# Optimization experiments

Measured on AMD Instinct MI355X. Metric: run time of the kernel, lower is better.

## Reference

```python
import jax, jax.numpy as jnp
import numpy as np

VOCAB, EMB, CAP, T, B, H, NC = 50000, 200, 3, 500, 128, 256, 6


def lstm_layer(x_seq, W, b):
    """TF LSTMCell (forget_bias=1.0, tanh) over x_seq [T,B,D] -> hs [T,B,H]."""
    Hh = b.shape[0] // 4
    Bn = x_seq.shape[1]
    def step(carry, x):
        c, h = carry
        z = jnp.concatenate([x, h], axis=-1) @ W + b  # [B,4H]
        i, j, f, o = jnp.split(z, 4, axis=-1)         # TF gate order i,j,f,o
        c = jax.nn.sigmoid(f + 1.0) * c + jax.nn.sigmoid(i) * jnp.tanh(j)
        h = jax.nn.sigmoid(o) * jnp.tanh(c)
        return (c, h), h
    init = (jnp.zeros((Bn, Hh), x_seq.dtype), jnp.zeros((Bn, Hh), x_seq.dtype))
    _, hs = jax.lax.scan(step, init, x_seq)
    return hs


def stack3(x_seq, Ws, bs):
    h = x_seq
    for W, b in zip(Ws, bs):  # fixed 3 layers
        h = lstm_layer(h, W, b)
    return h


def setup_inputs() -> dict:
    key = jax.random.key(0)
    ks = jax.random.split(key, 16)
    s = 0.05
    inp = {
        "words": jax.random.randint(ks[0], (B, T), 0, VOCAB, dtype=jnp.int32),
        "capitals": jax.random.randint(ks[1], (B, T), 0, 4, dtype=jnp.int32),
        "embed_words": jax.random.normal(ks[2], (VOCAB, EMB), jnp.float32) * s,
        "cap_table": jnp.concatenate([jnp.eye(CAP, dtype=jnp.float32),
                                       jnp.zeros((1, CAP), jnp.float32)], 0),
    }
    D0 = EMB + CAP + H  # 459
    D1 = H + H          # 512
    names = [("Wf0", D0), ("Wf1", D1), ("Wf2", D1), ("Wb0", D0), ("Wb1", D1), ("Wb2", D1)]
    for i, (nm, d) in enumerate(names):
        inp[nm] = jax.random.normal(ks[3 + i], (d, 4 * H), jnp.float32) * s
        inp["b" + nm[1:]] = jnp.zeros((4 * H,), jnp.float32)
    inp["d1_W"] = jax.random.normal(ks[10], (2 * H, 64), jnp.float32) * s
    inp["d1_b"] = jnp.zeros((64,), jnp.float32)
    inp["d2_W"] = jax.random.normal(ks[11], (64, NC), jnp.float32) * s
    inp["d2_b"] = jnp.zeros((NC,), jnp.float32)
    return inp


def reference(words, capitals, embed_words, cap_table,
              Wf0, bf0, Wf1, bf1, Wf2, bf2,
              Wb0, bb0, Wb1, bb1, Wb2, bb2,
              d1_W, d1_b, d2_W, d2_b):
    # embed + concat -> [B,T,203], then time-major [T,B,203]
    x = jnp.concatenate([embed_words[words], cap_table[capitals]], axis=-1)
    x = jnp.transpose(x, (1, 0, 2))
    hf = stack3(x, (Wf0, Wf1, Wf2), (bf0, bf1, bf2))                     # [T,B,H]
    hb = stack3(x[::-1], (Wb0, Wb1, Wb2), (bb0, bb1, bb2))[::-1]         # [T,B,H]
    rnn_out = jnp.max(jnp.concatenate([hf, hb], axis=-1), axis=0)        # [B,2H]
    h1 = jax.nn.elu(rnn_out @ d1_W + d1_b)
    return jax.nn.sigmoid(h1 @ d2_W + d2_b)                              # [B,NC]
```

## Files before the change

### kernel.cpp

```cpp
#include <hip/hip_runtime.h>
#include <stdint.h>

#define TSTEPS 500
#define NB 128
#define NH 256
#define RINGN 8

typedef _Float16 f16;
typedef _Float16 f16x8 __attribute__((ext_vector_type(8)));
typedef float f32x4 __attribute__((ext_vector_type(4)));
typedef unsigned long long u64;
typedef unsigned int u32;

static constexpr size_t HSLOT = (size_t)NB*NH;
static constexpr size_t SZ_XCAT  = (size_t)TSTEPS*NB*256*2;
static constexpr size_t SZ_WLDS  = (size_t)6*4*256*256*2;
static constexpr size_t SZ_WREG  = (size_t)6*4*4*4*8*64*8*2;
static constexpr size_t SZ_BIAS  = (size_t)6*4*256*4;
static constexpr size_t SZ_HNEXT = (size_t)6*RINGN*HSLOT*2;
static constexpr size_t SZ_HLOC  = (size_t)6*RINGN*HSLOT*2;
static constexpr size_t SZ_FLAG  = (size_t)6*(TSTEPS+1)*16*4;
static constexpr size_t SZ_DONE  = 256;
static constexpr size_t SZ_RNN   = (size_t)NB*512*4;
static constexpr size_t OFF_XCAT  = 0;
static constexpr size_t OFF_WLDS  = OFF_XCAT + SZ_XCAT;
static constexpr size_t OFF_WREG  = OFF_WLDS + SZ_WLDS;
static constexpr size_t OFF_BIAS  = OFF_WREG + SZ_WREG;
static constexpr size_t OFF_HNEXT = OFF_BIAS + SZ_BIAS;
static constexpr size_t OFF_HLOC  = OFF_HNEXT + SZ_HNEXT;
static constexpr size_t OFF_FLAGL = OFF_HLOC + SZ_HLOC;
static constexpr size_t OFF_FLAGN = OFF_FLAGL + SZ_FLAG;
static constexpr size_t OFF_DONE  = OFF_FLAGN + SZ_FLAG;
static constexpr size_t OFF_RNN   = (OFF_DONE + SZ_DONE + 255) & ~(size_t)255;
static constexpr size_t WS_NEED   = OFF_RNN + SZ_RNN;

__global__ void embed_kernel(const int* __restrict__ words,
                             const int* __restrict__ caps,
                             const float* __restrict__ emb,
                             const float* __restrict__ capt,
                             f16* __restrict__ xcat) {
  int t = blockIdx.x >> 7, b = blockIdx.x & 127, k = threadIdx.x;
  int w  = words[b*TSTEPS + t];
  int cp = caps [b*TSTEPS + t];
  float v = 0.f;
  if (k < 200)      v = emb[(size_t)w*200 + k];
  else if (k < 203) v = capt[cp*3 + (k-200)];
  xcat[((size_t)t*NB + b)*256 + k] = (f16)v;
}

__global__ void pack_kernel(const float* __restrict__ Wf0, const float* __restrict__ bf0,
                            const float* __restrict__ Wf1, const float* __restrict__ bf1,
                            const float* __restrict__ Wf2, const float* __restrict__ bf2,
                            const float* __restrict__ Wb0, const float* __restrict__ bb0,
                            const float* __restrict__ Wb1, const float* __restrict__ bb1,
                            const float* __restrict__ Wb2, const float* __restrict__ bb2,
                            f16* __restrict__ wlds, f16* __restrict__ wreg,
                            float* __restrict__ bias) {
  int bid = blockIdx.x;
  int layer;
  const float* W; const float* bb;
  int part1 = (bid < 6144);
  if (part1) layer = bid >> 10;
  else       layer = (bid - 6144) >> 6;
  switch (layer) {
    case 0: W = Wf0; bb = bf0; break;
    case 1: W = Wf1; bb = bf1; break;
    case 2: W = Wf2; bb = bf2; break;
    case 3: W = Wb0; bb = bb0; break;
    case 4: W = Wb1; bb = bb1; break;
    default: W = Wb2; bb = bb2; break;
  }
  int level = layer % 3;
  if (part1) {
    int ug = (bid >> 8) & 3;
    int n = bid & 255;
    int g = n >> 6, u = n & 63;
    int col = g*256 + ug*64 + u;
    if (threadIdx.x == 0)
      bias[(size_t)(layer*4 + ug)*256 + n] = bb[col] + (g == 2 ? 1.f : 0.f);
    int k = threadIdx.x;
    int row = (level == 0) ? ((k < 203) ? k : -1) : k;
    float v = (row < 0) ? 0.f : W[(size_t)row*1024 + col];
    int idx = (((k >> 3) ^ (n & 7)) << 3) | (k & 7);
    wlds[((size_t)(layer*4 + ug)*256 + n)*256 + idx] = (f16)v;
  } else {
    int r2 = (bid - 6144) & 63;
    int ug = r2 >> 4, wv = (r2 >> 2) & 3, g = r2 & 3;
    int lane = threadIdx.x & 63;
    int col = g*256 + ug*64 + wv*16 + (lane & 15);
    int rbase = (level == 0) ? 203 : 256;
    for (int ks = threadIdx.x >> 6; ks < 8; ks += 4) {
      size_t base = ((((size_t)(layer*4 + ug)*4 + wv)*4 + g)*8 + ks)*512 + (size_t)lane*8;
      #pragma unroll
      for (int j = 0; j < 8; ++j) {
        int k = ks*32 + ((lane >> 4)*8) + j;
        wreg[base + j] = (f16)W[(size_t)(rbase + k)*1024 + col];
      }
    }
  }
}

__global__ void init_kernel(int* __restrict__ flagL, int* __restrict__ flagN,
                            f16* __restrict__ hnext, int* __restrict__ done) {
  int i = blockIdx.x*256 + threadIdx.x;
  if (i < 6*(TSTEPS+1)*16) {
    int t = (i >> 4) % (TSTEPS+1);
    flagL[i] = 0;
    flagN[i] = (t == 0) ? 9 : 0;
  }
  if (i < 98304) {
    int l = i >> 14, e = i & 16383;
    ((u32*)(hnext + (size_t)l*RINGN*HSLOT))[e] = 0u;
  }
  if (i == 0) *done = 0;
}

__device__ __forceinline__ int poll_agent(const int* q) {
  int v;
  for (;;) {
    v = __hip_atomic_load(q, __ATOMIC_RELAXED, __HIP_MEMORY_SCOPE_AGENT);
    if (__all(v != 0)) break;
    __builtin_amdgcn_s_sleep(1);
  }
  return v;
}
__device__ __forceinline__ int ld_flag_l(const int* p) {
  int v;
  asm volatile("global_load_dword %0, %1, off sc0\n\ts_waitcnt vmcnt(0)"
               : "=v"(v) : "v"(p) : "memory");
  return v;
}
__device__ __forceinline__ f16x8 ld_a_l(const f16* p) {
  f16x8 v;
  asm volatile("global_load_dwordx4 %0, %1, off sc0" : "=v"(v) : "v"(p));
  return v;
}
__device__ __forceinline__ f16x8 ld_a_p(const f16* p) {
  f16x8 v;
  asm volatile("global_load_dwordx4 %0, %1, off" : "=v"(v) : "v"(p));
  return v;
}
__device__ __forceinline__ f16x8 ldA_coh(const f16* p) {
  union { u64 q[2]; f16x8 v; } u;
  u.q[0] = __hip_atomic_load((const u64*)p,     __ATOMIC_RELAXED, __HIP_MEMORY_SCOPE_AGENT);
  u.q[1] = __hip_atomic_load((const u64*)p + 1, __ATOMIC_RELAXED, __HIP_MEMORY_SCOPE_AGENT);
  return u.v;
}
__device__ __forceinline__ void st_h_l(f16* p, short s) {
  asm volatile("global_store_short %0, %1, off" :: "v"(p), "v"((int)s) : "memory");
}
__device__ __forceinline__ void st_flag_plain(int* p, int v) {
  asm volatile("global_store_dword %0, %1, off" :: "v"(p), "v"(v) : "memory");
}
__device__ __forceinline__ void vm_wait(int n) {
  if (n == 0)      asm volatile("s_waitcnt vmcnt(0)" ::: "memory");
  else if (n == 8) asm volatile("s_waitcnt vmcnt(8)" ::: "memory");
  __builtin_amdgcn_sched_barrier(0);
}
__device__ __forceinline__ float sigf(float x) {
  return __builtin_amdgcn_rcpf(1.f + __expf(-x));
}
__device__ __forceinline__ float tanhf_(float x) {
  float e = __expf(-2.f*fabsf(x));
  float r = (1.f - e) * __builtin_amdgcn_rcpf(1.f + e);
  return x < 0.f ? -r : r;
}

__global__ __launch_bounds__(256, 1)
void lstm_pipeline(const f16* __restrict__ xcat, const f16* __restrict__ wlds,
                   const f16* __restrict__ wreg, const float* __restrict__ bias,
                   f16* hnext, f16* hloc, int* flagL, int* flagN, int* done,
                   float* __restrict__ rnn_out) {
  const int bid = blockIdx.x;
  const int layer = bid & 7, sub = bid >> 3;
  if (bid >= 128 || layer >= 6) {
    f16x8 ha;
    #pragma unroll
    for (int j = 0; j < 8; ++j) ha[j] = (f16)1.0f;
    f32x4 hc0 = (f32x4){0,0,0,0}, hc1 = (f32x4){0,0,0,0};
    f32x4 hc2 = (f32x4){0,0,0,0}, hc3 = (f32x4){0,0,0,0};
    for (u32 it = 0;; ++it) {
      #pragma unroll
      for (int j = 0; j < 16; ++j) {
        hc0 = __builtin_amdgcn_mfma_f32_16x16x32_f16(ha, ha, hc0, 0,0,0);
        hc1 = __builtin_amdgcn_mfma_f32_16x16x32_f16(ha, ha, hc1, 0,0,0);
        hc2 = __builtin_amdgcn_mfma_f32_16x16x32_f16(ha, ha, hc2, 0,0,0);
        hc3 = __builtin_amdgcn_mfma_f32_16x16x32_f16(ha, ha, hc3, 0,0,0);
      }
      if ((it & 31) == 31) {
        if (__hip_atomic_load(done, __ATOMIC_RELAXED, __HIP_MEMORY_SCOPE_AGENT) >= 96)
          break;
      }
    }
    asm volatile("" :: "v"(hc0), "v"(hc1), "v"(hc2), "v"(hc3));
    return;
  }
  const int rg = sub >> 2, ug = sub & 3;
  extern __shared__ char smem[];
  const int stack = layer/3, level = layer - stack*3;

  {
    const uint4* src = (const uint4*)(wlds + (size_t)(layer*4 + ug)*256*256);
    uint4* dst = (uint4*)smem;
    for (int i = threadIdx.x; i < 8192; i += 256) dst[i] = src[i];
  }
  const int lane = threadIdx.x & 63, wv = threadIdx.x >> 6;
  const int lc = lane & 15, akg = lane >> 4;
  const int slot4 = rg*4 + (lane & 3);
  const int xcp1 = ((int)__builtin_amdgcn_s_getreg((31 << 11) | 20) & 7) + 1;

  f16x8 Brec[4][8];
  {
    const f16* wr = wreg + ((size_t)(layer*4 + ug)*4 + wv)*4*8*512;
    #pragma unroll
    for (int g = 0; g < 4; ++g)
      #pragma unroll
      for (int ks = 0; ks < 8; ++ks)
        Brec[g][ks] = *(const f16x8*)(wr + ((size_t)(g*8 + ks)*64 + lane)*8);
  }
  float bI, bJ, bF, bO;
  {
    const float* bb = bias + (size_t)(layer*4 + ug)*256 + wv*16 + lc;
    bI = bb[0*64]; bJ = bb[1*64]; bF = bb[2*64]; bO = bb[3*64];
  }
  __syncthreads();

  const size_t FL = (size_t)(TSTEPS+1)*16;
  int*       flL  = flagL + (size_t)layer*FL;
  int*       flN  = flagN + (size_t)layer*FL;
  const int* flNp = flagN + (size_t)(layer-1)*FL;
  const int* flNn = flagN + (size_t)(layer+1)*FL;

  const size_t aoff = (size_t)(rg*32 + lc)*256 + (size_t)akg*8;
  const int ucol = ug*64 + wv*16 + lc;

  float c_st[2][4], hmx[2][4];
  #pragma unroll
  for (int mt = 0; mt < 2; ++mt)
    #pragma unroll
    for (int r = 0; r < 4; ++r) { c_st[mt][r] = 0.f; hmx[mt][r] = -2.f; }

  f16x8 aI[2][8];
  f32x4 acc[2][4];
  int prev_ok = 0;
  bool prev_l2 = false;

#define LOAD_AI(T)                                                                    \
  do {                                                                                \
    if (level == 0) {                                                                 \
      const f16* A_ = xcat + (size_t)(stack ? (TSTEPS - (T)) : ((T)-1))*NB*256;       \
      _Pragma("unroll")                                                               \
      for (int mt = 0; mt < 2; ++mt)                                                  \
        _Pragma("unroll")                                                             \
        for (int ks = 0; ks < 8; ++ks)                                                \
          aI[mt][ks] = ld_a_p(A_ + aoff + mt*4096 + ks*32);                           \
    } else if (prev_l2) {                                                             \
      const f16* A_ = hloc + ((size_t)(layer-1)*RINGN + (size_t)((T) & 7))*HSLOT;     \
      _Pragma("unroll")                                                               \
      for (int mt = 0; mt < 2; ++mt)                                                  \
        _Pragma("unroll")                                                             \
        for (int ks = 0; ks < 8; ++ks)                                                \
          aI[mt][ks] = ld_a_l(A_ + aoff + mt*4096 + ks*32);                           \
    } else {                                                                          \
      const f16* A_ = hnext + ((size_t)(layer-1)*RINGN + (size_t)((T) & 7))*HSLOT;    \
      _Pragma("unroll")                                                               \
      for (int mt = 0; mt < 2; ++mt)                                                  \
        _Pragma("unroll")                                                             \
        for (int ks = 0; ks < 8; ++ks)                                                \
          aI[mt][ks] = ldA_coh(A_ + aoff + mt*4096 + ks*32);                          \
    }                                                                                 \
  } while (0)

#define IN_GEMM()                                                                     \
  do {                                                                                \
    _Pragma("unroll")                                                                 \
    for (int mt = 0; mt < 2; ++mt)                                                    \
      _Pragma("unroll")                                                               \
      for (int g = 0; g < 4; ++g) acc[mt][g] = (f32x4){0.f,0.f,0.f,0.f};              \
    _Pragma("unroll")                                                                 \
    for (int ks = 0; ks < 8; ++ks) {                                                  \
      const int swz = (((ks*4 + akg) ^ (lc & 7)) << 4);                               \
      f16x8 vb0 = *(const f16x8*)(smem + (0*64 + wv*16 + lc)*512 + swz);              \
      f16x8 vb1 = *(const f16x8*)(smem + (1*64 + wv*16 + lc)*512 + swz);              \
      f16x8 vb2 = *(const f16x8*)(smem + (2*64 + wv*16 + lc)*512 + swz);              \
      f16x8 vb3 = *(const f16x8*)(smem + (3*64 + wv*16 + lc)*512 + swz);              \
      _Pragma("unroll")                                                               \
      for (int mt = 0; mt < 2; ++mt) {                                                \
        acc[mt][0] = __builtin_amdgcn_mfma_f32_16x16x32_f16(aI[mt][ks], vb0, acc[mt][0],0,0,0); \
        acc[mt][1] = __builtin_amdgcn_mfma_f32_16x16x32_f16(aI[mt][ks], vb1, acc[mt][1],0,0,0); \
        acc[mt][2] = __builtin_amdgcn_mfma_f32_16x16x32_f16(aI[mt][ks], vb2, acc[mt][2],0,0,0); \
        acc[mt][3] = __builtin_amdgcn_mfma_f32_16x16x32_f16(aI[mt][ks], vb3, acc[mt][3],0,0,0); \
      }                                                                               \
    }                                                                                 \
  } while (0)

  if (level) {
    int la = 4 > TSTEPS ? TSTEPS : 4;
    int v = poll_agent(flNp + (size_t)la*16 + slot4);
    prev_l2 = __all(v == xcp1);
    prev_ok = la;
  }
  LOAD_AI(1);
  vm_wait(0);
  IN_GEMM();

  for (int t = 1; t <= TSTEPS; ++t) {
    bool fast;
    {
      const int* qL = flL + (size_t)(t-1)*16 + slot4;
      const int* qN = flN + (size_t)(t-1)*16 + slot4;
      int it = 0;
      for (;;) {
        int vL = ld_flag_l(qL);
        if (__all(vL == xcp1)) { fast = true; break; }
        if ((++it & 3) == 0) {
          int vN = __hip_atomic_load(qN, __ATOMIC_RELAXED, __HIP_MEMORY_SCOPE_AGENT);
          if (__all(vN != 0)) { fast = false; break; }
        }
        __builtin_amdgcn_s_sleep(1);
      }
    }
    __builtin_amdgcn_sched_barrier(0);

    f16x8 aH[2][8];
    {
      const size_t hb = ((size_t)layer*RINGN + (size_t)((t-1) & 7))*HSLOT;
      if (fast) {
        const f16* A = hloc + hb;
        #pragma unroll
        for (int mt = 0; mt < 2; ++mt)
          #pragma unroll
          for (int ks = 0; ks < 8; ++ks)
            aH[mt][ks] = ld_a_l(A + aoff + mt*4096 + ks*32);
      } else {
        const f16* A = hnext + hb;
        #pragma unroll
        for (int mt = 0; mt < 2; ++mt)
          #pragma unroll
          for (int ks = 0; ks < 8; ++ks)
            aH[mt][ks] = ldA_coh(A + aoff + mt*4096 + ks*32);
      }
    }
    __builtin_amdgcn_sched_barrier(0);

    if (level < 2 && t >= 8 && (t & 1) == 0)
      poll_agent(flNn + (size_t)(t-6)*16 + slot4);
    if (level && t < TSTEPS && prev_ok < t + 1) {
      int la = (t + 4 <= TSTEPS) ? t + 4 : TSTEPS;
      int v = poll_agent(flNp + (size_t)la*16 + slot4);
      prev_l2 = __all(v == xcp1);
      prev_ok = la;
    }
    __builtin_amdgcn_sched_barrier(0);

    vm_wait(0);
    #pragma unroll
    for (int ks = 0; ks < 8; ++ks)
      #pragma unroll
      for (int mt = 0; mt < 2; ++mt) {
        acc[mt][0] = __builtin_amdgcn_mfma_f32_16x16x32_f16(aH[mt][ks], Brec[0][ks], acc[mt][0],0,0,0);
        acc[mt][1] = __builtin_amdgcn_mfma_f32_16x16x32_f16(aH[mt][ks], Brec[1][ks], acc[mt][1],0,0,0);
        acc[mt][2] = __builtin_amdgcn_mfma_f32_16x16x32_f16(aH[mt][ks], Brec[2][ks], acc[mt][2],0,0,0);
        acc[mt][3] = __builtin_amdgcn_mfma_f32_16x16x32_f16(aH[mt][ks], Brec[3][ks], acc[mt][3],0,0,0);
      }
    __builtin_amdgcn_sched_barrier(0);

    if (t < TSTEPS) LOAD_AI(t + 1);
    __builtin_amdgcn_sched_barrier(0);

    short hh[2][4];
    #pragma unroll
    for (int mt = 0; mt < 2; ++mt) {
      #pragma unroll
      for (int r = 0; r < 4; ++r) {
        float zi = acc[mt][0][r] + bI;
        float zj = acc[mt][1][r] + bJ;
        float zf = acc[mt][2][r] + bF;
        float zo = acc[mt][3][r] + bO;
        float cs = sigf(zf)*c_st[mt][r] + sigf(zi)*tanhf_(zj);
        c_st[mt][r] = cs;
        float h = sigf(zo)*tanhf_(cs);
        if (level == 2) hmx[mt][r] = fmaxf(hmx[mt][r], h);
        union { f16 h; short s; } cv; cv.h = (f16)h;
        hh[mt][r] = cv.s;
      }
    }

    {
      const size_t ob = ((size_t)layer*RINGN + (size_t)(t & 7))*HSLOT;
      f16* hl = hloc  + ob;
      f16* hn = hnext + ob;
      #pragma unroll
      for (int mt = 0; mt < 2; ++mt)
        #pragma unroll
        for (int r = 0; r < 4; ++r) {
          int row = rg*32 + mt*16 + akg*4 + r;
          st_h_l(hl + (size_t)row*256 + ucol, hh[mt][r]);
        }
      __builtin_amdgcn_sched_barrier(0);
      #pragma unroll
      for (int mt = 0; mt < 2; ++mt)
        #pragma unroll
        for (int r = 0; r < 4; ++r) {
          int row = rg*32 + mt*16 + akg*4 + r;
          __hip_atomic_store((short*)(hn + (size_t)row*256 + ucol), hh[mt][r],
                             __ATOMIC_RELAXED, __HIP_MEMORY_SCOPE_AGENT);
        }
      __builtin_amdgcn_sched_barrier(0);
    }

    vm_wait(8);
    __syncthreads();
    if (threadIdx.x == 0) st_flag_plain(flL + (size_t)t*16 + rg*4 + ug, xcp1);

    if (t < TSTEPS) IN_GEMM();

    vm_wait(0);
    __syncthreads();
    if (threadIdx.x == 0)
      __hip_atomic_store(flN + (size_t)t*16 + rg*4 + ug, xcp1,
                         __ATOMIC_RELAXED, __HIP_MEMORY_SCOPE_AGENT);
  }
#undef LOAD_AI
#undef IN_GEMM

  if (level == 2) {
    #pragma unroll
    for (int mt = 0; mt < 2; ++mt)
      #pragma unroll
      for (int r = 0; r < 4; ++r)
        rnn_out[(size_t)(rg*32 + mt*16 + akg*4 + r)*512 + stack*256 + ucol] = hmx[mt][r];
  }

  __syncthreads();
  if (threadIdx.x == 0)
    __hip_atomic_fetch_add(done, 1, __ATOMIC_RELAXED, __HIP_MEMORY_SCOPE_AGENT);
}

__global__ __launch_bounds__(256)
void dense_kernel(const float* __restrict__ rnn, const float* __restrict__ W1,
                  const float* __restrict__ b1, const float* __restrict__ W2,
                  const float* __restrict__ b2, float* __restrict__ out) {
  __shared__ float h1[16][64];
  int r0 = blockIdx.x*16;
  int c = threadIdx.x & 63, rr = threadIdx.x >> 6;
  #pragma unroll
  for (int m = 0; m < 4; ++m) {
    int rl = rr*4 + m;
    const float* rp = rnn + (size_t)(r0 + rl)*512;
    float s = b1[c];
    for (int k = 0; k < 512; ++k) s = fmaf(rp[k], W1[(size_t)k*64 + c], s);
    h1[rl][c] = (s > 0.f) ? s : (__expf(s) - 1.f);
  }
  __syncthreads();
  if (threadIdx.x < 96) {
    int rl = threadIdx.x/6, cc = threadIdx.x - rl*6;
    float s = b2[cc];
    #pragma unroll
    for (int k = 0; k < 64; ++k) s = fmaf(h1[rl][k], W2[k*6 + cc], s);
    out[(size_t)(r0 + rl)*6 + cc] = 1.f/(1.f + __expf(-s));
  }
}

extern "C" void kernel_launch(void* const* d_in, const int* in_sizes, int n_in,
                              void* d_out, int out_size, void* d_ws, size_t ws_size,
                              hipStream_t stream) {
  if (ws_size < WS_NEED) return;
  const int*   words = (const int*)d_in[0];
  const int*   caps  = (const int*)d_in[1];
  const float* emb   = (const float*)d_in[2];
  const float* capt  = (const float*)d_in[3];
  char* ws = (char*)d_ws;
  f16*   xcat  = (f16*)  (ws + OFF_XCAT);
  f16*   wlds  = (f16*)  (ws + OFF_WLDS);
  f16*   wreg  = (f16*)  (ws + OFF_WREG);
  float* bias  = (float*)(ws + OFF_BIAS);
  f16*   hnext = (f16*)  (ws + OFF_HNEXT);
  f16*   hloc  = (f16*)  (ws + OFF_HLOC);
  int*   flagL = (int*)  (ws + OFF_FLAGL);
  int*   flagN = (int*)  (ws + OFF_FLAGN);
  int*   done  = (int*)  (ws + OFF_DONE);
  float* rnn   = (float*)(ws + OFF_RNN);

  embed_kernel<<<TSTEPS*NB, 256, 0, stream>>>(words, caps, emb, capt, xcat);
  pack_kernel<<<6144 + 384, 256, 0, stream>>>(
      (const float*)d_in[4],  (const float*)d_in[5],  (const float*)d_in[6],  (const float*)d_in[7],
      (const float*)d_in[8],  (const float*)d_in[9],  (const float*)d_in[10], (const float*)d_in[11],
      (const float*)d_in[12], (const float*)d_in[13], (const float*)d_in[14], (const float*)d_in[15],
      wlds, wreg, bias);
  init_kernel<<<768, 256, 0, stream>>>(flagL, flagN, hnext, done);
  lstm_pipeline<<<256, 256, 131072, stream>>>(xcat, wlds, wreg, bias, hnext, hloc,
                                              flagL, flagN, done, rnn);
  dense_kernel<<<8, 256, 0, stream>>>(rnn, (const float*)d_in[16], (const float*)d_in[17],
                                      (const float*)d_in[18], (const float*)d_in[19], (float*)d_out);
}
```

Baseline: 3.889 ms.

## Move neighbor-flag polling to end of step; replace MFMA spinner with integer xorshift

The poll of neighbouring layers' progress flags moves from between the h-load and the recurrent MFMA to the end of the previous iteration, so the flag wait overlaps the tail of that step instead of sitting on the critical path. The idle filler blocks, which keep the clock up while the real blocks work, now spin on integer xorshift ALU work instead of MFMA, and they check the done counter more often. The intent is to cut per-step latency and to stop the filler from competing for matrix units or power. The risk is that flag visibility timing changes relative to the loads issued at the top of the next step.

```diff
diff --git a/kernel.cpp b/kernel.cpp
--- a/kernel.cpp
+++ b/kernel.cpp
@@ -165,6 +165,9 @@
   float r = (1.f - e) * __builtin_amdgcn_rcpf(1.f + e);
   return x < 0.f ? -r : r;
 }
+__device__ __forceinline__ u32 xs(u32 x) {
+  x ^= x << 13; x ^= x >> 17; x ^= x << 5; return x;
+}
 
 __global__ __launch_bounds__(256, 1)
 void lstm_pipeline(const f16* __restrict__ xcat, const f16* __restrict__ wlds,
@@ -174,25 +177,22 @@
   const int bid = blockIdx.x;
   const int layer = bid & 7, sub = bid >> 3;
   if (bid >= 128 || layer >= 6) {
-    f16x8 ha;
-    #pragma unroll
-    for (int j = 0; j < 8; ++j) ha[j] = (f16)1.0f;
-    f32x4 hc0 = (f32x4){0,0,0,0}, hc1 = (f32x4){0,0,0,0};
-    f32x4 hc2 = (f32x4){0,0,0,0}, hc3 = (f32x4){0,0,0,0};
+    u32 h0 = bid*2654435761u + threadIdx.x + 1, h1 = h0 ^ 0x9E3779B9u, h2 = h0 + 77u,
+        h3 = h1 + 13u, h4 = h0 ^ 0x85EBCA6Bu, h5 = h1 ^ 0xC2B2AE35u, h6 = h2 ^ 7u,
+        h7 = h3 ^ 0x27D4EB2Fu;
     for (u32 it = 0;; ++it) {
       #pragma unroll
-      for (int j = 0; j < 16; ++j) {
-        hc0 = __builtin_amdgcn_mfma_f32_16x16x32_f16(ha, ha, hc0, 0,0,0);
-        hc1 = __builtin_amdgcn_mfma_f32_16x16x32_f16(ha, ha, hc1, 0,0,0);
-        hc2 = __builtin_amdgcn_mfma_f32_16x16x32_f16(ha, ha, hc2, 0,0,0);
-        hc3 = __builtin_amdgcn_mfma_f32_16x16x32_f16(ha, ha, hc3, 0,0,0);
-      }
-      if ((it & 31) == 31) {
+      for (int j = 0; j < 8; ++j) {
+        h0 = xs(h0); h1 = xs(h1); h2 = xs(h2); h3 = xs(h3);
+        h4 = xs(h4); h5 = xs(h5); h6 = xs(h6); h7 = xs(h7);
+      }
+      if ((it & 7) == 7) {
         if (__hip_atomic_load(done, __ATOMIC_RELAXED, __HIP_MEMORY_SCOPE_AGENT) >= 96)
           break;
       }
     }
-    asm volatile("" :: "v"(hc0), "v"(hc1), "v"(hc2), "v"(hc3));
+    asm volatile("" :: "v"(h0), "v"(h1), "v"(h2), "v"(h3),
+                       "v"(h4), "v"(h5), "v"(h6), "v"(h7));
     return;
   }
   const int rg = sub >> 2, ug = sub & 3;
@@ -343,16 +343,6 @@
     }
     __builtin_amdgcn_sched_barrier(0);
 
-    if (level < 2 && t >= 8 && (t & 1) == 0)
-      poll_agent(flNn + (size_t)(t-6)*16 + slot4);
-    if (level && t < TSTEPS && prev_ok < t + 1) {
-      int la = (t + 4 <= TSTEPS) ? t + 4 : TSTEPS;
-      int v = poll_agent(flNp + (size_t)la*16 + slot4);
-      prev_l2 = __all(v == xcp1);
-      prev_ok = la;
-    }
-    __builtin_amdgcn_sched_barrier(0);
-
     vm_wait(0);
     #pragma unroll
     for (int ks = 0; ks < 8; ++ks)
@@ -420,6 +410,18 @@
     if (threadIdx.x == 0)
       __hip_atomic_store(flN + (size_t)t*16 + rg*4 + ug, xcp1,
                          __ATOMIC_RELAXED, __HIP_MEMORY_SCOPE_AGENT);
+
+    if (t < TSTEPS) {
+      const int tn = t + 1;
+      if (level < 2 && tn >= 8 && (tn & 1) == 0)
+        poll_agent(flNn + (size_t)(tn-6)*16 + slot4);
+      if (level && prev_ok < tn + 1) {
+        int la = (tn + 4 <= TSTEPS) ? tn + 4 : TSTEPS;
+        int v = poll_agent(flNp + (size_t)la*16 + slot4);
+        prev_l2 = __all(v == xcp1);
+        prev_ok = la;
+      }
+    }
   }
 #undef LOAD_AI
 #undef IN_GEMM
```

Result: no change. 3.962 ms (+1.9%).
